# Performance work log

Hardware: AMD Instinct MI355X
Metric: run time of the kernel (lower is better)

## Reference

```python
import jax, jax.numpy as jnp
import numpy as np

NEG_SLOPE = 0.01  # F.leaky_relu default
EPS = 1e-12       # F.normalize default eps

def _lrelu(h):
    return jnp.where(h > 0, h, NEG_SLOPE * h)

def setup_inputs() -> dict:
    key = jax.random.key(0)
    ks = jax.random.split(key, 16)
    N, E, D = 100000, 800000, 64
    x = jax.random.normal(ks[0], (N, D), dtype=jnp.float32)
    src = jax.random.randint(ks[1], (E,), 0, N, dtype=jnp.int32)
    dst = jax.random.randint(ks[2], (E,), 0, N, dtype=jnp.int32)
    def lin(k, fo, fi):
        k1, k2 = jax.random.split(k)
        s = 1.0 / np.sqrt(fi)
        w = jax.random.uniform(k1, (fo, fi), jnp.float32, -s, s)
        b = jax.random.uniform(k2, (fo,), jnp.float32, -s, s)
        return w, b
    w1, b1 = lin(ks[3], 256, D)
    w2, b2 = lin(ks[4], 128, 256)
    w3, b3 = lin(ks[5], 64, 128)
    w4, b4 = lin(ks[6], 1, 64)
    w_self, _ = lin(ks[7], D, D)   # SAGEConv fc_self (no bias)
    w_neigh, _ = lin(ks[8], D, D)  # SAGEConv fc_neigh (no bias)
    bias = jnp.zeros((D,), jnp.float32)  # SAGEConv bias param
    return dict(x=x, src=src, dst=dst, w1=w1, b1=b1, w2=w2, b2=b2,
                w3=w3, b3=b3, w4=w4, b4=b4,
                w_self=w_self, w_neigh=w_neigh, bias=bias)

def reference(x, src, dst, w1, b1, w2, b2, w3, b3, w4, b4, w_self, w_neigh, bias):
    N = x.shape[0]
    # per-edge score MLP on (h_u - h_v)
    d = x[src] - x[dst]                       # [E, D]
    h = _lrelu(d @ w1.T + b1)                 # [E, 256]
    h = _lrelu(h @ w2.T + b2)                 # [E, 128]
    h = _lrelu(h @ w3.T + b3)                 # [E, 64]
    e = jax.nn.sigmoid(h @ w4.T + b4)         # [E, 1]
    # SAGEConv 'mean' with edge weights: mean over incoming edges of e * x_src
    msg = e * x[src]                          # [E, D]
    s = jax.ops.segment_sum(msg, dst, num_segments=N)               # [N, D]
    deg = jax.ops.segment_sum(jnp.ones((src.shape[0],), x.dtype), dst,
                              num_segments=N)                        # [N]
    neigh = s / jnp.maximum(deg, 1.0)[:, None]
    A = x @ w_self.T + neigh @ w_neigh.T + bias
    A = _lrelu(A)
    norm = jnp.maximum(jnp.linalg.norm(A, axis=1, keepdims=True), EPS)
    A = A / norm
    return A, e
```

## Files before the change

kernel.cpp:

```cpp
#include <hip/hip_runtime.h>

typedef unsigned short u16;
typedef unsigned int   u32;
typedef __attribute__((ext_vector_type(8))) short short8;
typedef __attribute__((ext_vector_type(4))) float f32x4;

__device__ __forceinline__ u16 f2bf(float f) {
  u32 u = __float_as_uint(f);
  u += 0x7FFFu + ((u >> 16) & 1u);
  return (u16)(u >> 16);
}
__device__ __forceinline__ float bf2f(u16 h) { return __uint_as_float(((u32)h) << 16); }
__device__ __forceinline__ u32 pk2(float lo, float hi) {
  return (u32)f2bf(lo) | ((u32)f2bf(hi) << 16);
}
__device__ __forceinline__ float lrelu(float v) { return v > 0.f ? v : 0.01f * v; }

__host__ __device__ __forceinline__ int sig(int c) {
  return ((c >> 5) << 5) | ((c & 12) << 1) | (((c >> 4) & 1) << 2) | (c & 3);
}

union U8 { u32 w[4]; short8 v; };

#define MFMA16(A, B, C) __builtin_amdgcn_mfma_f32_16x16x32_bf16(A, B, C, 0, 0, 0)

#define W2_BASE 2048
#define W3_BASE 6144
#define NCHUNK8 7168


__global__ __launch_bounds__(512, 2) void edge_mlp(
    const float* __restrict__ x, const int* __restrict__ src, const int* __restrict__ dst,
    const short8* __restrict__ wcat,
    const float* __restrict__ b1p, const float* __restrict__ b2p, const float* __restrict__ b3p,
    const float* __restrict__ w4p, const float* __restrict__ b4,
    const int* __restrict__ rowptr, int* __restrict__ cursor,
    u16* __restrict__ msgbuf, float* __restrict__ eout, int E)
{
  __shared__ short8 ldsw[NCHUNK8];
  const int tid  = threadIdx.x;
  const int lane = tid & 63;
  const int wv   = tid >> 6;
  const int g    = lane >> 4;
  const int r    = lane & 15;
  const int eb   = (blockIdx.x * 8 + wv) * 32;
  const int e0   = eb + r, e1 = eb + 16 + r;
  const int ec0  = e0 < E ? e0 : E - 1;
  const int ec1  = e1 < E ? e1 : E - 1;
  const int sn0 = src[ec0], dn0 = dst[ec0];
  const int sn1 = src[ec1], dn1 = dst[ec1];
  const float b4v = b4[0];

  const float* xsr0 = x + (size_t)sn0 * 64 + 8 * g;
  const float* xdr0 = x + (size_t)dn0 * 64 + 8 * g;
  const float* xsr1 = x + (size_t)sn1 * 64 + 8 * g;
  const float* xdr1 = x + (size_t)dn1 * 64 + 8 * g;
  const float4 a0s0 = *(const float4*)(xsr0),      a0s1 = *(const float4*)(xsr0 + 4);
  const float4 a0s2 = *(const float4*)(xsr0 + 32), a0s3 = *(const float4*)(xsr0 + 36);
  const float4 a0d0 = *(const float4*)(xdr0),      a0d1 = *(const float4*)(xdr0 + 4);
  const float4 a0d2 = *(const float4*)(xdr0 + 32), a0d3 = *(const float4*)(xdr0 + 36);
  const float4 a1s0 = *(const float4*)(xsr1),      a1s1 = *(const float4*)(xsr1 + 4);
  const float4 a1s2 = *(const float4*)(xsr1 + 32), a1s3 = *(const float4*)(xsr1 + 36);
  const float4 a1d0 = *(const float4*)(xdr1),      a1d1 = *(const float4*)(xdr1 + 4);
  const float4 a1d2 = *(const float4*)(xdr1 + 32), a1d3 = *(const float4*)(xdr1 + 36);

  {
    const short8* gp = wcat + wv * 64 + lane;
    short8*       lp = ldsw + wv * 64;
#pragma unroll
    for (int i = 0; i < 14; i++) {
      __builtin_amdgcn_global_load_lds(
          (const __attribute__((address_space(1))) u32*)(gp + i * 512),
          (__attribute__((address_space(3))) u32*)(lp + i * 512), 16, 0, 0);
    }
  }
  __syncthreads();

  U8 bA0, bB0, bA1, bB1;
  bA0.w[0] = pk2(a0s0.x - a0d0.x, a0s0.y - a0d0.y);
  bA0.w[1] = pk2(a0s0.z - a0d0.z, a0s0.w - a0d0.w);
  bA0.w[2] = pk2(a0s1.x - a0d1.x, a0s1.y - a0d1.y);
  bA0.w[3] = pk2(a0s1.z - a0d1.z, a0s1.w - a0d1.w);
  bB0.w[0] = pk2(a0s2.x - a0d2.x, a0s2.y - a0d2.y);
  bB0.w[1] = pk2(a0s2.z - a0d2.z, a0s2.w - a0d2.w);
  bB0.w[2] = pk2(a0s3.x - a0d3.x, a0s3.y - a0d3.y);
  bB0.w[3] = pk2(a0s3.z - a0d3.z, a0s3.w - a0d3.w);
  bA1.w[0] = pk2(a1s0.x - a1d0.x, a1s0.y - a1d0.y);
  bA1.w[1] = pk2(a1s0.z - a1d0.z, a1s0.w - a1d0.w);
  bA1.w[2] = pk2(a1s1.x - a1d1.x, a1s1.y - a1d1.y);
  bA1.w[3] = pk2(a1s1.z - a1d1.z, a1s1.w - a1d1.w);
  bB1.w[0] = pk2(a1s2.x - a1d2.x, a1s2.y - a1d2.y);
  bB1.w[1] = pk2(a1s2.z - a1d2.z, a1s2.w - a1d2.w);
  bB1.w[2] = pk2(a1s3.x - a1d3.x, a1s3.y - a1d3.y);
  bB1.w[3] = pk2(a1s3.z - a1d3.z, a1s3.w - a1d3.w);

  u32 h1a[32], h1b[32];
  {
    const float* b1l = b1p + 4 * g;
#pragma unroll
    for (int t = 0; t < 16; t++) {
      short8 a0 = ldsw[(t * 2 + 0) * 64 + lane];
      short8 a1 = ldsw[(t * 2 + 1) * 64 + lane];
      f32x4 p = {}, q = {};
      p = MFMA16(a0, bA0.v, p); p = MFMA16(a1, bB0.v, p);
      q = MFMA16(a0, bA1.v, q); q = MFMA16(a1, bB1.v, q);
      float4 bb = *(const float4*)(b1l + 16 * t);
      h1a[2 * t]     = pk2(lrelu(p[0] + bb.x), lrelu(p[1] + bb.y));
      h1a[2 * t + 1] = pk2(lrelu(p[2] + bb.z), lrelu(p[3] + bb.w));
      h1b[2 * t]     = pk2(lrelu(q[0] + bb.x), lrelu(q[1] + bb.y));
      h1b[2 * t + 1] = pk2(lrelu(q[2] + bb.z), lrelu(q[3] + bb.w));
    }
  }

  u32 h2a[16], h2b[16];
  {
    const float* b2l = b2p + 4 * g;
#pragma unroll
    for (int t = 0; t < 8; t++) {
      f32x4 p = {}, q = {};
#pragma unroll
      for (int s = 0; s < 8; s++) {
        short8 a = ldsw[W2_BASE + (t * 8 + s) * 64 + lane];
        U8 f0, f1;
        f0.w[0] = h1a[4 * s + 0]; f0.w[1] = h1a[4 * s + 1];
        f0.w[2] = h1a[4 * s + 2]; f0.w[3] = h1a[4 * s + 3];
        f1.w[0] = h1b[4 * s + 0]; f1.w[1] = h1b[4 * s + 1];
        f1.w[2] = h1b[4 * s + 2]; f1.w[3] = h1b[4 * s + 3];
        p = MFMA16(a, f0.v, p);
        q = MFMA16(a, f1.v, q);
      }
      float4 bb = *(const float4*)(b2l + 16 * t);
      h2a[2 * t]     = pk2(lrelu(p[0] + bb.x), lrelu(p[1] + bb.y));
      h2a[2 * t + 1] = pk2(lrelu(p[2] + bb.z), lrelu(p[3] + bb.w));
      h2b[2 * t]     = pk2(lrelu(q[0] + bb.x), lrelu(q[1] + bb.y));
      h2b[2 * t + 1] = pk2(lrelu(q[2] + bb.z), lrelu(q[3] + bb.w));
    }
  }

  float dot0 = 0.f, dot1 = 0.f;
  {
    const float* b3l = b3p + 4 * g;
    const float* w4l = w4p + 4 * g;
#pragma unroll
    for (int t = 0; t < 4; t++) {
      f32x4 p = {}, q = {};
#pragma unroll
      for (int s = 0; s < 4; s++) {
        short8 a = ldsw[W3_BASE + (t * 4 + s) * 64 + lane];
        U8 f0, f1;
        f0.w[0] = h2a[4 * s + 0]; f0.w[1] = h2a[4 * s + 1];
        f0.w[2] = h2a[4 * s + 2]; f0.w[3] = h2a[4 * s + 3];
        f1.w[0] = h2b[4 * s + 0]; f1.w[1] = h2b[4 * s + 1];
        f1.w[2] = h2b[4 * s + 2]; f1.w[3] = h2b[4 * s + 3];
        p = MFMA16(a, f0.v, p);
        q = MFMA16(a, f1.v, q);
      }
      float4 bb = *(const float4*)(b3l + 16 * t);
      float4 ww = *(const float4*)(w4l + 16 * t);
      dot0 += lrelu(p[0] + bb.x) * ww.x + lrelu(p[1] + bb.y) * ww.y
            + lrelu(p[2] + bb.z) * ww.z + lrelu(p[3] + bb.w) * ww.w;
      dot1 += lrelu(q[0] + bb.x) * ww.x + lrelu(q[1] + bb.y) * ww.y
            + lrelu(q[2] + bb.z) * ww.z + lrelu(q[3] + bb.w) * ww.w;
    }
  }
  dot0 += __shfl_xor(dot0, 16); dot0 += __shfl_xor(dot0, 32);
  dot1 += __shfl_xor(dot1, 16); dot1 += __shfl_xor(dot1, 32);
  const float ev0 = 1.f / (1.f + __expf(-(dot0 + b4v)));
  const float ev1 = 1.f / (1.f + __expf(-(dot1 + b4v)));

  int pos0 = 0, pos1 = 0;
  if (g == 0) {
    if (e0 < E) { eout[e0] = ev0; pos0 = rowptr[dn0] + atomicAdd(&cursor[dn0], 1); }
    if (e1 < E) { eout[e1] = ev1; pos1 = rowptr[dn1] + atomicAdd(&cursor[dn1], 1); }
  }
  pos0 = __shfl(pos0, r);
  pos1 = __shfl(pos1, r);
  if (e0 < E) {
    u16* mp = msgbuf + (size_t)pos0 * 64 + g * 16;
    union { u16 s[8]; short8 v; } m0, m1;
    m0.s[0] = f2bf(ev0 * a0s0.x); m0.s[1] = f2bf(ev0 * a0s0.y);
    m0.s[2] = f2bf(ev0 * a0s0.z); m0.s[3] = f2bf(ev0 * a0s0.w);
    m0.s[4] = f2bf(ev0 * a0s1.x); m0.s[5] = f2bf(ev0 * a0s1.y);
    m0.s[6] = f2bf(ev0 * a0s1.z); m0.s[7] = f2bf(ev0 * a0s1.w);
    m1.s[0] = f2bf(ev0 * a0s2.x); m1.s[1] = f2bf(ev0 * a0s2.y);
    m1.s[2] = f2bf(ev0 * a0s2.z); m1.s[3] = f2bf(ev0 * a0s2.w);
    m1.s[4] = f2bf(ev0 * a0s3.x); m1.s[5] = f2bf(ev0 * a0s3.y);
    m1.s[6] = f2bf(ev0 * a0s3.z); m1.s[7] = f2bf(ev0 * a0s3.w);
    *(short8*)(mp)     = m0.v;
    *(short8*)(mp + 8) = m1.v;
  }
  if (e1 < E) {
    u16* mp = msgbuf + (size_t)pos1 * 64 + g * 16;
    union { u16 s[8]; short8 v; } m0, m1;
    m0.s[0] = f2bf(ev1 * a1s0.x); m0.s[1] = f2bf(ev1 * a1s0.y);
    m0.s[2] = f2bf(ev1 * a1s0.z); m0.s[3] = f2bf(ev1 * a1s0.w);
    m0.s[4] = f2bf(ev1 * a1s1.x); m0.s[5] = f2bf(ev1 * a1s1.y);
    m0.s[6] = f2bf(ev1 * a1s1.z); m0.s[7] = f2bf(ev1 * a1s1.w);
    m1.s[0] = f2bf(ev1 * a1s2.x); m1.s[1] = f2bf(ev1 * a1s2.y);
    m1.s[2] = f2bf(ev1 * a1s2.z); m1.s[3] = f2bf(ev1 * a1s2.w);
    m1.s[4] = f2bf(ev1 * a1s3.x); m1.s[5] = f2bf(ev1 * a1s3.y);
    m1.s[6] = f2bf(ev1 * a1s3.z); m1.s[7] = f2bf(ev1 * a1s3.w);
    *(short8*)(mp)     = m0.v;
    *(short8*)(mp + 8) = m1.v;
  }
}

__global__ void deg_hist(const int* __restrict__ dst, int* __restrict__ degi, int E)
{
  const int i = blockIdx.x * 256 + threadIdx.x;
  if (i < E) atomicAdd(&degi[dst[i]], 1);
}

__global__ void scan_part(const int* __restrict__ degi, int* __restrict__ rowptr,
                          int* __restrict__ bsum, int N)
{
  __shared__ int wsum[4];
  const int tid = threadIdx.x, lane = tid & 63, w = tid >> 6;
  const int base = blockIdx.x * 1024 + tid * 4;
  int d0 = 0, d1 = 0, d2 = 0, d3 = 0;
  if (base + 3 < N) {
    int4 v = *(const int4*)(degi + base);
    d0 = v.x; d1 = v.y; d2 = v.z; d3 = v.w;
  } else {
    if (base < N)     d0 = degi[base];
    if (base + 1 < N) d1 = degi[base + 1];
    if (base + 2 < N) d2 = degi[base + 2];
    if (base + 3 < N) d3 = degi[base + 3];
  }
  const int ts = d0 + d1 + d2 + d3;
  int sc = ts;
#pragma unroll
  for (int o = 1; o < 64; o <<= 1) { int v = __shfl_up(sc, o); if (lane >= o) sc += v; }
  if (lane == 63) wsum[w] = sc;
  __syncthreads();
  int woff = 0;
  for (int i = 0; i < w; i++) woff += wsum[i];
  const int ex = woff + sc - ts;
  if (base < N)     rowptr[base]     = ex;
  if (base + 1 < N) rowptr[base + 1] = ex + d0;
  if (base + 2 < N) rowptr[base + 2] = ex + d0 + d1;
  if (base + 3 < N) rowptr[base + 3] = ex + d0 + d1 + d2;
  if (tid == 255) bsum[blockIdx.x] = woff + sc;
}

__global__ void scan_bsum(int* __restrict__ bsum, int nb)
{
  __shared__ int wsum[4];
  const int tid = threadIdx.x, lane = tid & 63, w = tid >> 6;
  const int v = tid < nb ? bsum[tid] : 0;
  int sc = v;
#pragma unroll
  for (int o = 1; o < 64; o <<= 1) { int t = __shfl_up(sc, o); if (lane >= o) sc += t; }
  if (lane == 63) wsum[w] = sc;
  __syncthreads();
  int woff = 0;
  for (int i = 0; i < w; i++) woff += wsum[i];
  if (tid < nb) bsum[tid] = woff + sc - v;
}

__global__ void scan_add(int* __restrict__ rowptr, const int* __restrict__ bsum,
                         int* __restrict__ cursor, int N, int E)
{
  const int base = blockIdx.x * 1024 + threadIdx.x * 4;
  const int off = bsum[blockIdx.x];
#pragma unroll
  for (int i = 0; i < 4; i++)
    if (base + i < N) { rowptr[base + i] += off; cursor[base + i] = 0; }
  if (blockIdx.x == 0 && threadIdx.x == 0) rowptr[N] = E;
}

__global__ __launch_bounds__(256, 4) void node_agg_mfma(
    const float* __restrict__ x, const u16* __restrict__ msgbuf,
    const int* __restrict__ rowptr, const short8* __restrict__ wfin,
    const float* __restrict__ bias, float* __restrict__ A, int N)
{
  __shared__ short8 ldsW[1024];
  __shared__ float  nbuf[4][16][68];
  const int tid = threadIdx.x, wv = tid >> 6, lane = tid & 63;
  const int g = lane >> 4, r = lane & 15;
  for (int i = tid; i < 1024; i += 256) ldsW[i] = wfin[i];

  const int n0 = (blockIdx.x * 4 + wv) * 16;
  const int nr = (n0 + r) < N ? (n0 + r) : N - 1;
  const float* xp = x + (size_t)nr * 64 + 8 * g;
  const float4 xf0 = *(const float4*)(xp);
  const float4 xf1 = *(const float4*)(xp + 4);
  const float4 xf2 = *(const float4*)(xp + 32);
  const float4 xf3 = *(const float4*)(xp + 36);
  int rp = 0;
  if (lane < 17) rp = rowptr[min(n0 + lane, N)];
  const int cch = (((lane >> 3) & 1) << 5) | ((lane >> 4) << 3) | (lane & 7);
  for (int rr = 0; rr < 16; rr++) {
    const int s = __shfl(rp, rr);
    const int t = __shfl(rp, rr + 1);
    float acc = 0.f;
    for (int j = s; j < t; j += 4) {
      const int j1 = (j + 1 < t) ? j + 1 : j;
      const int j2 = (j + 2 < t) ? j + 2 : j;
      const int j3 = (j + 3 < t) ? j + 3 : j;
      const float v0 = bf2f(msgbuf[(size_t)j  * 64 + lane]);
      const float v1 = bf2f(msgbuf[(size_t)j1 * 64 + lane]);
      const float v2 = bf2f(msgbuf[(size_t)j2 * 64 + lane]);
      const float v3 = bf2f(msgbuf[(size_t)j3 * 64 + lane]);
      const float m1 = (j + 1 < t) ? 1.f : 0.f;
      const float m2 = (j + 2 < t) ? 1.f : 0.f;
      const float m3 = (j + 3 < t) ? 1.f : 0.f;
      acc += v0 + m1 * v1 + m2 * v2 + m3 * v3;
    }
    const float inv = 1.f / fmaxf((float)(t - s), 1.f);
    nbuf[wv][rr][cch] = acc * inv;
  }
  __syncthreads();

  U8 bf0, bf1, bf2q, bf3q;
  bf0.w[0] = pk2(xf0.x, xf0.y); bf0.w[1] = pk2(xf0.z, xf0.w);
  bf0.w[2] = pk2(xf1.x, xf1.y); bf0.w[3] = pk2(xf1.z, xf1.w);
  bf1.w[0] = pk2(xf2.x, xf2.y); bf1.w[1] = pk2(xf2.z, xf2.w);
  bf1.w[2] = pk2(xf3.x, xf3.y); bf1.w[3] = pk2(xf3.z, xf3.w);
  {
    const float* nb = nbuf[wv][r];
    const float4 n0v = *(const float4*)(nb + 8 * g);
    const float4 n1v = *(const float4*)(nb + 8 * g + 4);
    const float4 n2v = *(const float4*)(nb + 32 + 8 * g);
    const float4 n3v = *(const float4*)(nb + 32 + 8 * g + 4);
    bf2q.w[0] = pk2(n0v.x, n0v.y); bf2q.w[1] = pk2(n0v.z, n0v.w);
    bf2q.w[2] = pk2(n1v.x, n1v.y); bf2q.w[3] = pk2(n1v.z, n1v.w);
    bf3q.w[0] = pk2(n2v.x, n2v.y); bf3q.w[1] = pk2(n2v.z, n2v.w);
    bf3q.w[2] = pk2(n3v.x, n3v.y); bf3q.w[3] = pk2(n3v.z, n3v.w);
  }

  f32x4 acct[4] = {};
#pragma unroll
  for (int t = 0; t < 4; t++) {
    acct[t] = MFMA16(ldsW[(t * 4 + 0) * 64 + lane], bf0.v,  acct[t]);
    acct[t] = MFMA16(ldsW[(t * 4 + 1) * 64 + lane], bf1.v,  acct[t]);
    acct[t] = MFMA16(ldsW[(t * 4 + 2) * 64 + lane], bf2q.v, acct[t]);
    acct[t] = MFMA16(ldsW[(t * 4 + 3) * 64 + lane], bf3q.v, acct[t]);
  }

  f32x4 av[4];
  float ss = 0.f;
#pragma unroll
  for (int t = 0; t < 4; t++) {
    const float4 bb = *(const float4*)(bias + 16 * t + 4 * g);
    av[t][0] = lrelu(acct[t][0] + bb.x);
    av[t][1] = lrelu(acct[t][1] + bb.y);
    av[t][2] = lrelu(acct[t][2] + bb.z);
    av[t][3] = lrelu(acct[t][3] + bb.w);
    ss += av[t][0] * av[t][0] + av[t][1] * av[t][1]
        + av[t][2] * av[t][2] + av[t][3] * av[t][3];
  }
  ss += __shfl_xor(ss, 16); ss += __shfl_xor(ss, 32);
  const float rn = 1.f / fmaxf(sqrtf(ss), 1e-12f);
  if (n0 + r < N) {
    float* ap = A + (size_t)(n0 + r) * 64 + 4 * g;
#pragma unroll
    for (int t = 0; t < 4; t++) {
      float4 o;
      o.x = av[t][0] * rn; o.y = av[t][1] * rn;
      o.z = av[t][2] * rn; o.w = av[t][3] * rn;
      *(float4*)(ap + 16 * t) = o;
    }
  }
}

__global__ void convert_w(const float* __restrict__ w1, const float* __restrict__ w2,
                          const float* __restrict__ w3,
                          const float* __restrict__ b1, const float* __restrict__ b2,
                          const float* __restrict__ b3, const float* __restrict__ w4,
                          const float* __restrict__ w_self, const float* __restrict__ w_neigh,
                          u16* __restrict__ wcat, u16* __restrict__ wfin,
                          float* __restrict__ b1p, float* __restrict__ b2p,
                          float* __restrict__ b3p, float* __restrict__ w4p)
{
  const int idx = blockIdx.x * 256 + threadIdx.x;
  if (idx < 57344) {
    const float* w; int K, nsteps, loc;
    if (idx < 16384)      { loc = idx;         w = w1; K = 64;  nsteps = 2; }
    else if (idx < 49152) { loc = idx - 16384; w = w2; K = 256; nsteps = 8; }
    else                  { loc = idx - 49152; w = w3; K = 128; nsteps = 4; }
    const int chunk = loc >> 9;
    const int lane  = (loc >> 3) & 63;
    const int j     = loc & 7;
    const int t = chunk / nsteps, s = chunk % nsteps;
    const int m = sig(t * 16 + (lane & 15));
    const int k = s * 32 + (lane >> 4) * 8 + j;
    wcat[idx] = f2bf(w[m * K + k]);
  } else if (idx < 65536) {
    const int o = idx - 57344;
    const int c = o >> 9, lane = (o >> 3) & 63, j = o & 7;
    const int t = c >> 2, s = c & 3;
    const int m = 16 * t + (lane & 15);
    const int k = 32 * s + ((lane >> 4) << 3) + j;
    wfin[o] = f2bf(k < 64 ? w_self[m * 64 + k] : w_neigh[m * 64 + (k - 64)]);
  }
  if (idx < 256) b1p[idx] = b1[sig(idx)];
  if (idx < 128) b2p[idx] = b2[sig(idx)];
  if (idx < 64)  { b3p[idx] = b3[sig(idx)]; w4p[idx] = w4[sig(idx)]; }
}

extern "C" void kernel_launch(void* const* d_in, const int* in_sizes, int n_in,
                              void* d_out, int out_size, void* d_ws, size_t ws_size,
                              hipStream_t stream)
{
  const float* x       = (const float*)d_in[0];
  const int*   src     = (const int*)d_in[1];
  const int*   dst     = (const int*)d_in[2];
  const float* w1      = (const float*)d_in[3];
  const float* b1      = (const float*)d_in[4];
  const float* w2      = (const float*)d_in[5];
  const float* b2      = (const float*)d_in[6];
  const float* w3      = (const float*)d_in[7];
  const float* b3      = (const float*)d_in[8];
  const float* w4      = (const float*)d_in[9];
  const float* b4      = (const float*)d_in[10];
  const float* w_self  = (const float*)d_in[11];
  const float* w_neigh = (const float*)d_in[12];
  const float* bias    = (const float*)d_in[13];

  const int N = in_sizes[0] / 64;
  const int E = in_sizes[1];

  float* A    = (float*)d_out;
  float* eout = (float*)d_out + (size_t)N * 64;

  char* ws = (char*)d_ws;
  size_t off = 0;
  auto alloc = [&](size_t bytes) {
    void* p = ws + off;
    off = (off + bytes + 255) & ~(size_t)255;
    return p;
  };
  int*    degi   = (int*)alloc((size_t)N * 4);
  int*    rowptr = (int*)alloc((size_t)(N + 1) * 4);
  int*    cursor = (int*)alloc((size_t)N * 4);
  int*    bsum   = (int*)alloc(1024 * 4);
  short8* wcat   = (short8*)alloc((size_t)57344 * 2);
  short8* wfin   = (short8*)alloc((size_t)8192 * 2);
  float*  b1p    = (float*)alloc(256 * 4);
  float*  b2p    = (float*)alloc(128 * 4);
  float*  b3p    = (float*)alloc(64 * 4);
  float*  w4p    = (float*)alloc(64 * 4);
  u16*    msgbuf = (u16*)alloc((size_t)E * 128);

  hipMemsetAsync(degi, 0, (size_t)N * sizeof(int), stream);

  convert_w<<<256, 256, 0, stream>>>(w1, w2, w3, b1, b2, b3, w4, w_self, w_neigh,
                                     (u16*)wcat, (u16*)wfin, b1p, b2p, b3p, w4p);

  deg_hist<<<(E + 255) / 256, 256, 0, stream>>>(dst, degi, E);

  const int nsb = (N + 1023) / 1024;
  scan_part<<<nsb, 256, 0, stream>>>(degi, rowptr, bsum, N);
  scan_bsum<<<1, 256, 0, stream>>>(bsum, nsb);
  scan_add<<<nsb, 256, 0, stream>>>(rowptr, bsum, cursor, N, E);

  const int nblk = (E + 255) / 256;
  edge_mlp<<<nblk, 512, 0, stream>>>(x, src, dst, wcat, b1p, b2p, b3p, w4p, b4,
                                     rowptr, cursor, msgbuf, eout, E);

  const int nblk2 = (N + 63) / 64;
  node_agg_mfma<<<nblk2, 256, 0, stream>>>(x, msgbuf, rowptr, wfin, bias, A, N);
}
```

Before: 317.8 us.

## Double edge_mlp block size and use packed hardware bf16 conversion

Raises the edge MLP block from 512 to 1024 threads, so each block covers 512 edges and the 114 KB LDS weight staging is shared by twice as many edges. Because LDS allows only one such block per CU, this also doubles the waves resident per CU. The manual round-to-nearest bf16 packing is replaced with the HIP __float22bfloat162_rn intrinsic, which may lower to a packed convert instruction, and message stores reuse one packing union. The main risk is the aggressive launch-bounds hint (1024, 4), which may squeeze the register budget and cause spills in this MFMA-heavy kernel.

```diff
diff --git a/kernel.cpp b/kernel.cpp
--- a/kernel.cpp
+++ b/kernel.cpp
@@ -1,4 +1,5 @@
 #include <hip/hip_runtime.h>
+#include <hip/hip_bf16.h>
 
 typedef unsigned short u16;
 typedef unsigned int   u32;
@@ -12,7 +13,9 @@
 }
 __device__ __forceinline__ float bf2f(u16 h) { return __uint_as_float(((u32)h) << 16); }
 __device__ __forceinline__ u32 pk2(float lo, float hi) {
-  return (u32)f2bf(lo) | ((u32)f2bf(hi) << 16);
+  union { __hip_bfloat162 h; u32 u; } c;
+  c.h = __float22bfloat162_rn(make_float2(lo, hi));
+  return c.u;
 }
 __device__ __forceinline__ float lrelu(float v) { return v > 0.f ? v : 0.01f * v; }
 
@@ -29,7 +32,7 @@
 #define NCHUNK8 7168
 
 
-__global__ __launch_bounds__(512, 2) void edge_mlp(
+__global__ __launch_bounds__(1024, 4) void edge_mlp(
     const float* __restrict__ x, const int* __restrict__ src, const int* __restrict__ dst,
     const short8* __restrict__ wcat,
     const float* __restrict__ b1p, const float* __restrict__ b2p, const float* __restrict__ b3p,
@@ -43,7 +46,7 @@
   const int wv   = tid >> 6;
   const int g    = lane >> 4;
   const int r    = lane & 15;
-  const int eb   = (blockIdx.x * 8 + wv) * 32;
+  const int eb   = (blockIdx.x * 16 + wv) * 32;
   const int e0   = eb + r, e1 = eb + 16 + r;
   const int ec0  = e0 < E ? e0 : E - 1;
   const int ec1  = e1 < E ? e1 : E - 1;
@@ -68,10 +71,10 @@
     const short8* gp = wcat + wv * 64 + lane;
     short8*       lp = ldsw + wv * 64;
 #pragma unroll
-    for (int i = 0; i < 14; i++) {
+    for (int i = 0; i < 7; i++) {
       __builtin_amdgcn_global_load_lds(
-          (const __attribute__((address_space(1))) u32*)(gp + i * 512),
-          (__attribute__((address_space(3))) u32*)(lp + i * 512), 16, 0, 0);
+          (const __attribute__((address_space(1))) u32*)(gp + i * 1024),
+          (__attribute__((address_space(3))) u32*)(lp + i * 1024), 16, 0, 0);
     }
   }
   __syncthreads();
@@ -177,31 +180,31 @@
   pos1 = __shfl(pos1, r);
   if (e0 < E) {
     u16* mp = msgbuf + (size_t)pos0 * 64 + g * 16;
-    union { u16 s[8]; short8 v; } m0, m1;
-    m0.s[0] = f2bf(ev0 * a0s0.x); m0.s[1] = f2bf(ev0 * a0s0.y);
-    m0.s[2] = f2bf(ev0 * a0s0.z); m0.s[3] = f2bf(ev0 * a0s0.w);
-    m0.s[4] = f2bf(ev0 * a0s1.x); m0.s[5] = f2bf(ev0 * a0s1.y);
-    m0.s[6] = f2bf(ev0 * a0s1.z); m0.s[7] = f2bf(ev0 * a0s1.w);
-    m1.s[0] = f2bf(ev0 * a0s2.x); m1.s[1] = f2bf(ev0 * a0s2.y);
-    m1.s[2] = f2bf(ev0 * a0s2.z); m1.s[3] = f2bf(ev0 * a0s2.w);
-    m1.s[4] = f2bf(ev0 * a0s3.x); m1.s[5] = f2bf(ev0 * a0s3.y);
-    m1.s[6] = f2bf(ev0 * a0s3.z); m1.s[7] = f2bf(ev0 * a0s3.w);
-    *(short8*)(mp)     = m0.v;
-    *(short8*)(mp + 8) = m1.v;
+    U8 m;
+    m.w[0] = pk2(ev0 * a0s0.x, ev0 * a0s0.y);
+    m.w[1] = pk2(ev0 * a0s0.z, ev0 * a0s0.w);
+    m.w[2] = pk2(ev0 * a0s1.x, ev0 * a0s1.y);
+    m.w[3] = pk2(ev0 * a0s1.z, ev0 * a0s1.w);
+    *(short8*)(mp) = m.v;
+    m.w[0] = pk2(ev0 * a0s2.x, ev0 * a0s2.y);
+    m.w[1] = pk2(ev0 * a0s2.z, ev0 * a0s2.w);
+    m.w[2] = pk2(ev0 * a0s3.x, ev0 * a0s3.y);
+    m.w[3] = pk2(ev0 * a0s3.z, ev0 * a0s3.w);
+    *(short8*)(mp + 8) = m.v;
   }
   if (e1 < E) {
     u16* mp = msgbuf + (size_t)pos1 * 64 + g * 16;
-    union { u16 s[8]; short8 v; } m0, m1;
-    m0.s[0] = f2bf(ev1 * a1s0.x); m0.s[1] = f2bf(ev1 * a1s0.y);
-    m0.s[2] = f2bf(ev1 * a1s0.z); m0.s[3] = f2bf(ev1 * a1s0.w);
-    m0.s[4] = f2bf(ev1 * a1s1.x); m0.s[5] = f2bf(ev1 * a1s1.y);
-    m0.s[6] = f2bf(ev1 * a1s1.z); m0.s[7] = f2bf(ev1 * a1s1.w);
-    m1.s[0] = f2bf(ev1 * a1s2.x); m1.s[1] = f2bf(ev1 * a1s2.y);
-    m1.s[2] = f2bf(ev1 * a1s2.z); m1.s[3] = f2bf(ev1 * a1s2.w);
-    m1.s[4] = f2bf(ev1 * a1s3.x); m1.s[5] = f2bf(ev1 * a1s3.y);
-    m1.s[6] = f2bf(ev1 * a1s3.z); m1.s[7] = f2bf(ev1 * a1s3.w);
-    *(short8*)(mp)     = m0.v;
-    *(short8*)(mp + 8) = m1.v;
+    U8 m;
+    m.w[0] = pk2(ev1 * a1s0.x, ev1 * a1s0.y);
+    m.w[1] = pk2(ev1 * a1s0.z, ev1 * a1s0.w);
+    m.w[2] = pk2(ev1 * a1s1.x, ev1 * a1s1.y);
+    m.w[3] = pk2(ev1 * a1s1.z, ev1 * a1s1.w);
+    *(short8*)(mp) = m.v;
+    m.w[0] = pk2(ev1 * a1s2.x, ev1 * a1s2.y);
+    m.w[1] = pk2(ev1 * a1s2.z, ev1 * a1s2.w);
+    m.w[2] = pk2(ev1 * a1s3.x, ev1 * a1s3.y);
+    m.w[3] = pk2(ev1 * a1s3.z, ev1 * a1s3.w);
+    *(short8*)(mp + 8) = m.v;
   }
 }
 
@@ -455,9 +458,9 @@
   scan_bsum<<<1, 256, 0, stream>>>(bsum, nsb);
   scan_add<<<nsb, 256, 0, stream>>>(rowptr, bsum, cursor, N, E);
 
-  const int nblk = (E + 255) / 256;
-  edge_mlp<<<nblk, 512, 0, stream>>>(x, src, dst, wcat, b1p, b2p, b3p, w4p, b4,
-                                     rowptr, cursor, msgbuf, eout, E);
+  const int nblk = (E + 511) / 512;
+  edge_mlp<<<nblk, 1024, 0, stream>>>(x, src, dst, wcat, b1p, b2p, b3p, w4p, b4,
+                                      rowptr, cursor, msgbuf, eout, E);
 
   const int nblk2 = (N + 63) / 64;
   node_agg_mfma<<<nblk2, 256, 0, stream>>>(x, msgbuf, rowptr, wfin, bias, A, N);
```

Result: slower. 337.8 us (+6.3%).
